# Performance work log

Measured on AMD Instinct MI355X. Metric: run time of the kernel, lower is better.

Reference implementation:

```python
import jax, jax.numpy as jnp
import numpy as np

CLUSTER_NUMBER = 32
SPACING = 2.0 / CLUSTER_NUMBER
GRID = np.linspace(-1.0, 1.0, CLUSTER_NUMBER + 1)  # 33 bin centers, matches torch.linspace


def _eye_bbox_mask(eyes_bool):
    """Replicates the per-sample bounding-box (with 15% pad applied as in the
    original code, including the double-pad quirk on y_max/x_max)."""
    H, W = eyes_bool.shape
    rows_any = jnp.any(eyes_bool, axis=1)
    cols_any = jnp.any(eyes_bool, axis=0)
    ry = jnp.arange(H, dtype=jnp.int32)
    rx = jnp.arange(W, dtype=jnp.int32)
    y_min0 = jnp.min(jnp.where(rows_any, ry, H))
    y_max0 = jnp.max(jnp.where(rows_any, ry, -1))
    x_min0 = jnp.min(jnp.where(cols_any, rx, W))
    x_max0 = jnp.max(jnp.where(cols_any, rx, -1))
    pad_y = (0.15 * (y_max0 - y_min0).astype(jnp.float32)).astype(jnp.int32)
    pad_x = (0.15 * (x_max0 - x_min0).astype(jnp.float32)).astype(jnp.int32)
    y_min = jnp.maximum(0, y_min0 - pad_y)
    y_max = jnp.minimum(H, y_max0 + pad_y)
    x_min = jnp.maximum(0, x_min0 - pad_x)
    x_max = jnp.minimum(W, x_max0 + pad_x)
    # original code pads y_max/x_max a second time
    y_max = jnp.minimum(H - 1, y_max + pad_y)
    x_max = jnp.minimum(W - 1, x_max + pad_x)
    m = ((ry >= y_min) & (ry < y_max))[:, None] & ((rx >= x_min) & (rx < x_max))[None, :]
    has_eyes = jnp.any(eyes_bool)
    return jnp.where(has_eyes, m, False).astype(jnp.float32)


def _region_masks(seg):
    # seg: [B,H,W] int labels
    lips = ((seg == 11) | (seg == 12)).astype(jnp.float32)
    face = (seg == 1).astype(jnp.float32)
    eyes_bool = (seg == 4) | (seg == 5)
    eye_shadow = jax.vmap(_eye_bbox_mask)(eyes_bool)
    return lips, face, eye_shadow


def _soft_hist(img, mask):
    """Masked soft histogram, equivalent to calc_hist over masked pixels.
    result[k] = sum_n m_n*relu(spacing - |g_k - x_n|) / (N * S)  (the *10 cancels).
    img: [B,C,H,W], mask: [B,H,W] -> hist [B,C,K+1], count N [B]."""
    m = mask[:, None]  # [B,1,H,W]
    # small fixed loop over 33 bins keeps the peak intermediate at one [B,C,H,W]
    num = jnp.stack(
        [jnp.sum(jnp.maximum(SPACING - jnp.abs(img - float(g)), 0.0) * m, axis=(2, 3))
         for g in GRID], axis=-1)  # [B,C,K+1]
    N = jnp.sum(mask, axis=(1, 2))  # [B]
    S = jnp.sum(num, axis=-1)       # [B,C]
    denom = N[:, None, None] * S[:, :, None]
    return num / jnp.where(denom > 0, denom, 1.0), N


def reference(gen_makeup, real_makeup, seg_gen, seg_real):
    B, C, H, W = gen_makeup.shape
    gen_regions = _region_masks(seg_gen)
    ref_regions = _region_masks(seg_real)
    weights = (1.0, 0.1, 1.0)  # lips, face, eyes
    total = jnp.zeros((), dtype=gen_makeup.dtype)
    for w, mg, mr in zip(weights, gen_regions, ref_regions):
        hg, ng = _soft_hist(gen_makeup, mg)
        hr, nr = _soft_hist(real_makeup, mr)
        l1 = jnp.mean(jnp.abs(hg - hr), axis=-1)  # [B,C]
        valid = ((ng > 0) & (nr > 0))[:, None]    # empty-region skip
        total = total + w * jnp.sum(jnp.where(valid, l1, 0.0))
    return total / (B * C * 3)


def setup_inputs() -> dict:
    key = jax.random.key(0)
    k1, k2, k3, k4 = jax.random.split(key, 4)
    B, C, H, W = 4, 3, 512, 512
    # images normalized to [-1,1] as in the GAN pipeline
    gen_makeup = jax.random.uniform(k1, (B, C, H, W), dtype=jnp.float32) * 2.0 - 1.0
    real_makeup = jax.random.uniform(k2, (B, C, H, W), dtype=jnp.float32) * 2.0 - 1.0
    seg_gen = jax.random.randint(k3, (B, H, W), 0, 19, dtype=jnp.int32)
    seg_real = jax.random.randint(k4, (B, H, W), 0, 19, dtype=jnp.int32)
    return {"gen_makeup": gen_makeup, "real_makeup": real_makeup,
            "seg_gen": seg_gen, "seg_real": seg_real}
```

## Files before the change

### kernel.cpp

```cpp
#include <hip/hip_runtime.h>

#define HH 512
#define WW 512
#define NB 4
#define NC 3
#define NK 33
#define SPC 0.0625f
#define REP 4
#define NREP 16
#define NCLS 7
#define CLS_SZ (NCLS*NC*NK)
#define GRP_SZ (3*NC*NK)
#define BBOX_CH 64
#define HIST_CH 128
#define NBLK_BBOX (2*NB*BBOX_CH)
#define NBLK_HIST (2*NB*HIST_CH)

#define BBP_OFF    0
#define GCNT_OFF   2056
#define GCNT_SZ    (REP*2*NB*GRP_SZ)
#define GSUM_OFF   (GCNT_OFF + GCNT_SZ)
#define WS_TOTAL   (GSUM_OFF + GCNT_SZ)
#define ZERO_BASE  2048
#define ZERO_SZ    (WS_TOTAL - ZERO_BASE)
#define ZERO_PER   ((ZERO_SZ + NBLK_BBOX - 1) / NBLK_BBOX)

__global__ __launch_bounds__(256) void k_bbox(const int* __restrict__ seg_gen,
                                              const int* __restrict__ seg_real,
                                              int* __restrict__ ws) {
    int bid = blockIdx.x, tid = (int)threadIdx.x;

    int zbase = ZERO_BASE + bid * ZERO_PER;
    for (int i = tid; i < ZERO_PER; i += 256) {
        int idx = zbase + i;
        if (idx < WS_TOTAL) ws[idx] = 0;
    }

    int map = bid / (NB * BBOX_CH);
    int rem = bid % (NB * BBOX_CH);
    int b = rem / BBOX_CH, chunk = rem % BBOX_CH;
    const int4* seg4 = (const int4*)((map == 0 ? seg_gen : seg_real) + b * HH * WW);
    int base4 = chunk * (4096 / 4);

    int4 v[4];
    #pragma unroll
    for (int it = 0; it < 4; ++it) v[it] = seg4[base4 + it * 256 + tid];

    int ymin = HH, ymax = -1, xmin = WW, xmax = -1;
    #pragma unroll
    for (int it = 0; it < 4; ++it) {
        int p0 = (base4 + it * 256 + tid) * 4;
        int h = p0 >> 9, w0 = p0 & (WW - 1);
        int sv[4] = {v[it].x, v[it].y, v[it].z, v[it].w};
        #pragma unroll
        for (int j = 0; j < 4; ++j) {
            int s = sv[j];
            if (s == 4 || s == 5) {
                ymin = min(ymin, h); ymax = max(ymax, h);
                xmin = min(xmin, w0 + j); xmax = max(xmax, w0 + j);
            }
        }
    }
    __shared__ int sy0[256], sy1[256], sx0[256], sx1[256];
    sy0[tid] = ymin; sy1[tid] = ymax; sx0[tid] = xmin; sx1[tid] = xmax;
    __syncthreads();
    for (int off = 128; off > 0; off >>= 1) {
        if (tid < off) {
            sy0[tid] = min(sy0[tid], sy0[tid + off]);
            sy1[tid] = max(sy1[tid], sy1[tid + off]);
            sx0[tid] = min(sx0[tid], sx0[tid + off]);
            sx1[tid] = max(sx1[tid], sx1[tid + off]);
        }
        __syncthreads();
    }
    if (tid == 0)
        ((int4*)ws)[BBP_OFF / 4 + bid] = make_int4(sy0[0], sy1[0], sx0[0], sx1[0]);
}

__global__ __launch_bounds__(256) void k_hist(const float* __restrict__ gen,
                                              const float* __restrict__ realv,
                                              const int* __restrict__ seg_gen,
                                              const int* __restrict__ seg_real,
                                              int* __restrict__ ws) {
    int bid = blockIdx.x, tid = (int)threadIdx.x;
    int map = bid / (NB * HIST_CH);
    int rem = bid % (NB * HIST_CH);
    int b = rem / HIST_CH, chunk = rem % HIST_CH;
    const float* img = (map == 0 ? gen : realv);
    const int* seg = (map == 0 ? seg_gen : seg_real) + b * HH * WW;

    __shared__ unsigned lh[NREP * CLS_SZ];
    __shared__ int sbb[5];

    for (int i = tid; i < NREP * CLS_SZ; i += 256) lh[i] = 0u;

    if (tid < 64) {
        int4 v = ((const int4*)ws)[BBP_OFF / 4 + (map * NB + b) * BBOX_CH + tid];
        #pragma unroll
        for (int off = 32; off > 0; off >>= 1) {
            v.x = min(v.x, __shfl_xor(v.x, off));
            v.y = max(v.y, __shfl_xor(v.y, off));
            v.z = min(v.z, __shfl_xor(v.z, off));
            v.w = max(v.w, __shfl_xor(v.w, off));
        }
        if (tid == 0) {
            int ymin0 = v.x, ymax0 = v.y, xmin0 = v.z, xmax0 = v.w;
            int has = (ymax0 >= 0);
            int pady = (int)(0.15f * (float)(ymax0 - ymin0));
            int padx = (int)(0.15f * (float)(xmax0 - xmin0));
            int ymin = max(0, ymin0 - pady);
            int ymaxv = min(HH, ymax0 + pady);
            int xminv = max(0, xmin0 - padx);
            int xmaxv = min(WW, xmax0 + padx);
            ymaxv = min(HH - 1, ymaxv + pady);
            xmaxv = min(WW - 1, xmaxv + padx);
            sbb[0] = ymin; sbb[1] = ymaxv; sbb[2] = xminv; sbb[3] = xmaxv; sbb[4] = has;
        }
    }
    __syncthreads();
    int bbym = sbb[0], bbyM = sbb[1], bbxm = sbb[2], bbxM = sbb[3], has = sbb[4];

    unsigned* lhr = lh + (tid & (NREP - 1)) * CLS_SZ;
    int q0 = chunk * (2048 / 4) + tid;
    int q1 = q0 + 256;
    const int4* seg4 = (const int4*)seg;
    int4 sA = seg4[q0], sB = seg4[q1];
    const float4* i4 = (const float4*)img + ((size_t)(b * NC) << 16);
    float4 fA0 = i4[(0 << 16) + q0], fA1 = i4[(1 << 16) + q0], fA2 = i4[(2 << 16) + q0];
    float4 fB0 = i4[(0 << 16) + q1], fB1 = i4[(1 << 16) + q1], fB2 = i4[(2 << 16) + q1];

    #pragma unroll
    for (int g = 0; g < 2; ++g) {
        int p = (g == 0 ? q0 : q1) * 4;
        int4 s4 = (g == 0) ? sA : sB;
        float xs0[4], xs1[4], xs2[4];
        { float4 f = (g == 0) ? fA0 : fB0; xs0[0]=f.x; xs0[1]=f.y; xs0[2]=f.z; xs0[3]=f.w; }
        { float4 f = (g == 0) ? fA1 : fB1; xs1[0]=f.x; xs1[1]=f.y; xs1[2]=f.z; xs1[3]=f.w; }
        { float4 f = (g == 0) ? fA2 : fB2; xs2[0]=f.x; xs2[1]=f.y; xs2[2]=f.z; xs2[3]=f.w; }
        int h = p >> 9, w0 = p & (WW - 1);
        bool eyerow = has && (h >= bbym) && (h < bbyM);
        int sv[4] = {s4.x, s4.y, s4.z, s4.w};
        #pragma unroll
        for (int j = 0; j < 4; ++j) {
            int s = sv[j];
            int cls = (int)((s == 11) | (s == 12))
                    | ((int)(s == 1) << 1)
                    | ((int)(eyerow & ((w0 + j) >= bbxm) & ((w0 + j) < bbxM)) << 2);
            if (!cls) continue;
            unsigned* basep = lhr + (cls - 1) * (NC * NK);
            #pragma unroll
            for (int c = 0; c < NC; ++c) {
                float x = (c == 0) ? xs0[j] : (c == 1) ? xs1[j] : xs2[j];
                float t = (x + 1.0f) * 16.0f;
                int k0 = (int)t;
                k0 = min(max(k0, 0), NK - 1);
                float f = t - (float)k0;
                unsigned pk = 0x1000000u | (unsigned)(f * 4096.0f);
                atomicAdd(&basep[c * NK + k0], pk);
            }
        }
    }
    __syncthreads();

    for (int i = tid; i < CLS_SZ; i += 256) {
        unsigned cnt = 0, fq = 0;
        #pragma unroll
        for (int r = 0; r < NREP; ++r) {
            unsigned v = lh[r * CLS_SZ + i];
            cnt += v >> 24;
            fq  += v & 0xFFFFFFu;
        }
        lh[i] = cnt;
        lh[CLS_SZ + i] = fq;
    }
    __syncthreads();

    int rep = bid & (REP - 1);
    unsigned* gcnt = (unsigned*)ws + GCNT_OFF + ((rep * 2 + map) * NB + b) * GRP_SZ;
    float*    gsum = (float*)ws + GSUM_OFF + ((rep * 2 + map) * NB + b) * GRP_SZ;
    const int rcls0[3] = {1, 2, 4};
    for (int i = tid; i < GRP_SZ; i += 256) {
        int r = i / (NC * NK);
        int rest = i % (NC * NK);
        unsigned cnt = 0, fq = 0;
        #pragma unroll
        for (int m = 1; m < 8; ++m) {
            if (m & rcls0[r]) {
                cnt += lh[(m - 1) * (NC * NK) + rest];
                fq  += lh[CLS_SZ + (m - 1) * (NC * NK) + rest];
            }
        }
        if (cnt) {
            atomicAdd(&gcnt[i], cnt);
            atomicAdd(&gsum[i], (float)fq * (1.0f / 4096.0f));
        }
    }
}

#define NITEM (2 * NB * GRP_SZ)
__global__ __launch_bounds__(1024) void k_final(const unsigned* __restrict__ wsu,
                                                const float* __restrict__ wsf,
                                                float* __restrict__ out) {
    int tid = (int)threadIdx.x;
    __shared__ float sC[NITEM], sF[NITEM], sNum[NITEM];
    __shared__ int   sN[2 * NB * 3];
    __shared__ float sS[2 * NB * NC * 3];
    __shared__ double sRed[1024];

    const unsigned* gcntAll = wsu + GCNT_OFF;
    const float*    gsumAll = wsf + GSUM_OFF;
    for (int i = tid; i < NITEM; i += 1024) {
        int mp = i / (NB * GRP_SZ);
        int r2 = i % (NB * GRP_SZ);
        int b2 = r2 / GRP_SZ, idx = r2 % GRP_SZ;
        float C = 0.0f, F = 0.0f;
        #pragma unroll
        for (int rp = 0; rp < REP; ++rp) {
            int off = ((rp * 2 + mp) * NB + b2) * GRP_SZ + idx;
            C += (float)gcntAll[off];
            F += gsumAll[off];
        }
        sC[i] = C; sF[i] = F;
    }
    __syncthreads();
    if (tid < 24) {
        int mp = tid / 12, b2 = (tid / 3) % NB, r = tid % 3;
        const float* p = sC + (mp * NB + b2) * GRP_SZ + r * (NC * NK);
        float n = 0.0f;
        for (int k = 0; k < NK; ++k) n += p[k];
        sN[tid] = (int)(n + 0.5f);
    }
    for (int i = tid; i < NITEM; i += 1024) {
        int k = i % NK;
        float fp = (k > 0) ? sF[i - 1] : 0.0f;
        sNum[i] = fmaxf(SPC * ((sC[i] - sF[i]) + fp), 0.0f);
    }
    __syncthreads();
    if (tid < 72) {
        float s = 0.0f;
        const float* p = sNum + tid * NK;
        for (int k = 0; k < NK; ++k) s += p[k];
        sS[tid] = s;
    }
    __syncthreads();
    double acc = 0.0;
    for (int j = tid; j < NB * GRP_SZ; j += 1024) {
        int b2 = j / GRP_SZ, idx = j % GRP_SZ;
        int r = idx / (NC * NK);
        int c = (idx / NK) % NC;
        int ng = sN[b2 * 3 + r];
        int nr = sN[12 + b2 * 3 + r];
        if (ng > 0 && nr > 0) {
            int g = b2 * 9 + r * 3 + c;
            float dg = (float)ng * sS[g];
            float dr = (float)nr * sS[36 + g];
            dg = (dg > 0.0f) ? dg : 1.0f;
            dr = (dr > 0.0f) ? dr : 1.0f;
            double d = fabs((double)(sNum[j] / dg) - (double)(sNum[NB * GRP_SZ + j] / dr));
            acc += ((r == 1) ? 0.1 : 1.0) * d;
        }
    }
    sRed[tid] = acc;
    __syncthreads();
    for (int off = 512; off > 0; off >>= 1) {
        if (tid < off) sRed[tid] += sRed[tid + off];
        __syncthreads();
    }
    if (tid == 0) out[0] = (float)(sRed[0] / (double)NK / (double)(NB * NC * 3));
}

extern "C" void kernel_launch(void* const* d_in, const int* in_sizes, int n_in,
                              void* d_out, int out_size, void* d_ws, size_t ws_size,
                              hipStream_t stream) {
    const float* gen    = (const float*)d_in[0];
    const float* realv  = (const float*)d_in[1];
    const int* seg_gen  = (const int*)d_in[2];
    const int* seg_real = (const int*)d_in[3];
    int* wsi = (int*)d_ws;

    k_bbox <<<dim3(NBLK_BBOX), dim3(256),  0, stream>>>(seg_gen, seg_real, wsi);
    k_hist <<<dim3(NBLK_HIST), dim3(256),  0, stream>>>(gen, realv, seg_gen, seg_real, wsi);
    k_final<<<dim3(1),         dim3(1024), 0, stream>>>((const unsigned*)d_ws,
                                                        (const float*)d_ws,
                                                        (float*)d_out);
}
```

Baseline: 28.61 us.

## Halve LDS histogram replicas, double bbox blocks, interleave replica partials for vector reads

Cuts the shared-memory histogram replicas from 16 to 8 and repacks counts and fractions into 12/20 bits, with fractions quantized to 512 levels instead of 4096. This shrinks LDS use and the per-block clear and reduction work. The bbox pass now uses twice as many blocks, each reading half the data, so the histogram kernel reads two partials per lane. The global replica partials are interleaved so the final kernel can sum them with single vector loads. The coarser fraction quantization lowers accuracy, and fewer replicas may raise LDS atomic contention.

```diff
diff --git a/kernel.cpp b/kernel.cpp
--- a/kernel.cpp
+++ b/kernel.cpp
@@ -7,21 +7,21 @@
 #define NK 33
 #define SPC 0.0625f
 #define REP 4
-#define NREP 16
+#define NREP 8
 #define NCLS 7
 #define CLS_SZ (NCLS*NC*NK)
 #define GRP_SZ (3*NC*NK)
-#define BBOX_CH 64
+#define BBOX_CH 128
 #define HIST_CH 128
 #define NBLK_BBOX (2*NB*BBOX_CH)
 #define NBLK_HIST (2*NB*HIST_CH)
 
 #define BBP_OFF    0
-#define GCNT_OFF   2056
-#define GCNT_SZ    (REP*2*NB*GRP_SZ)
+#define GCNT_OFF   4096
+#define GCNT_SZ    (2*NB*GRP_SZ*REP)
 #define GSUM_OFF   (GCNT_OFF + GCNT_SZ)
 #define WS_TOTAL   (GSUM_OFF + GCNT_SZ)
-#define ZERO_BASE  2048
+#define ZERO_BASE  GCNT_OFF
 #define ZERO_SZ    (WS_TOTAL - ZERO_BASE)
 #define ZERO_PER   ((ZERO_SZ + NBLK_BBOX - 1) / NBLK_BBOX)
 
@@ -40,18 +40,18 @@
     int rem = bid % (NB * BBOX_CH);
     int b = rem / BBOX_CH, chunk = rem % BBOX_CH;
     const int4* seg4 = (const int4*)((map == 0 ? seg_gen : seg_real) + b * HH * WW);
-    int base4 = chunk * (4096 / 4);
-
-    int4 v[4];
-    #pragma unroll
-    for (int it = 0; it < 4; ++it) v[it] = seg4[base4 + it * 256 + tid];
+    int base4 = chunk * 512;
+
+    int4 v0 = seg4[base4 + tid];
+    int4 v1 = seg4[base4 + 256 + tid];
 
     int ymin = HH, ymax = -1, xmin = WW, xmax = -1;
     #pragma unroll
-    for (int it = 0; it < 4; ++it) {
+    for (int it = 0; it < 2; ++it) {
         int p0 = (base4 + it * 256 + tid) * 4;
         int h = p0 >> 9, w0 = p0 & (WW - 1);
-        int sv[4] = {v[it].x, v[it].y, v[it].z, v[it].w};
+        int4 v = (it == 0) ? v0 : v1;
+        int sv[4] = {v.x, v.y, v.z, v.w};
         #pragma unroll
         for (int j = 0; j < 4; ++j) {
             int s = sv[j];
@@ -95,16 +95,19 @@
     for (int i = tid; i < NREP * CLS_SZ; i += 256) lh[i] = 0u;
 
     if (tid < 64) {
-        int4 v = ((const int4*)ws)[BBP_OFF / 4 + (map * NB + b) * BBOX_CH + tid];
+        const int4* bbp = (const int4*)ws + BBP_OFF / 4 + (map * NB + b) * BBOX_CH;
+        int4 a = bbp[tid], c = bbp[tid + 64];
+        a.x = min(a.x, c.x); a.y = max(a.y, c.y);
+        a.z = min(a.z, c.z); a.w = max(a.w, c.w);
         #pragma unroll
         for (int off = 32; off > 0; off >>= 1) {
-            v.x = min(v.x, __shfl_xor(v.x, off));
-            v.y = max(v.y, __shfl_xor(v.y, off));
-            v.z = min(v.z, __shfl_xor(v.z, off));
-            v.w = max(v.w, __shfl_xor(v.w, off));
+            a.x = min(a.x, __shfl_xor(a.x, off));
+            a.y = max(a.y, __shfl_xor(a.y, off));
+            a.z = min(a.z, __shfl_xor(a.z, off));
+            a.w = max(a.w, __shfl_xor(a.w, off));
         }
         if (tid == 0) {
-            int ymin0 = v.x, ymax0 = v.y, xmin0 = v.z, xmax0 = v.w;
+            int ymin0 = a.x, ymax0 = a.y, xmin0 = a.z, xmax0 = a.w;
             int has = (ymax0 >= 0);
             int pady = (int)(0.15f * (float)(ymax0 - ymin0));
             int padx = (int)(0.15f * (float)(xmax0 - xmin0));
@@ -121,7 +124,7 @@
     int bbym = sbb[0], bbyM = sbb[1], bbxm = sbb[2], bbxM = sbb[3], has = sbb[4];
 
     unsigned* lhr = lh + (tid & (NREP - 1)) * CLS_SZ;
-    int q0 = chunk * (2048 / 4) + tid;
+    int q0 = chunk * 512 + tid;
     int q1 = q0 + 256;
     const int4* seg4 = (const int4*)seg;
     int4 sA = seg4[q0], sB = seg4[q1];
@@ -155,7 +158,7 @@
                 int k0 = (int)t;
                 k0 = min(max(k0, 0), NK - 1);
                 float f = t - (float)k0;
-                unsigned pk = 0x1000000u | (unsigned)(f * 4096.0f);
+                unsigned pk = 0x100000u | (unsigned)(f * 512.0f);
                 atomicAdd(&basep[c * NK + k0], pk);
             }
         }
@@ -167,8 +170,8 @@
         #pragma unroll
         for (int r = 0; r < NREP; ++r) {
             unsigned v = lh[r * CLS_SZ + i];
-            cnt += v >> 24;
-            fq  += v & 0xFFFFFFu;
+            cnt += v >> 20;
+            fq  += v & 0xFFFFFu;
         }
         lh[i] = cnt;
         lh[CLS_SZ + i] = fq;
@@ -176,8 +179,8 @@
     __syncthreads();
 
     int rep = bid & (REP - 1);
-    unsigned* gcnt = (unsigned*)ws + GCNT_OFF + ((rep * 2 + map) * NB + b) * GRP_SZ;
-    float*    gsum = (float*)ws + GSUM_OFF + ((rep * 2 + map) * NB + b) * GRP_SZ;
+    unsigned* gcnt = (unsigned*)ws + GCNT_OFF + (map * NB + b) * GRP_SZ * REP;
+    float*    gsum = (float*)ws + GSUM_OFF + (map * NB + b) * GRP_SZ * REP;
     const int rcls0[3] = {1, 2, 4};
     for (int i = tid; i < GRP_SZ; i += 256) {
         int r = i / (NC * NK);
@@ -191,8 +194,8 @@
             }
         }
         if (cnt) {
-            atomicAdd(&gcnt[i], cnt);
-            atomicAdd(&gsum[i], (float)fq * (1.0f / 4096.0f));
+            atomicAdd(&gcnt[i * REP + rep], cnt);
+            atomicAdd(&gsum[i * REP + rep], (float)fq * (1.0f / 512.0f));
         }
     }
 }
@@ -210,17 +213,10 @@
     const unsigned* gcntAll = wsu + GCNT_OFF;
     const float*    gsumAll = wsf + GSUM_OFF;
     for (int i = tid; i < NITEM; i += 1024) {
-        int mp = i / (NB * GRP_SZ);
-        int r2 = i % (NB * GRP_SZ);
-        int b2 = r2 / GRP_SZ, idx = r2 % GRP_SZ;
-        float C = 0.0f, F = 0.0f;
-        #pragma unroll
-        for (int rp = 0; rp < REP; ++rp) {
-            int off = ((rp * 2 + mp) * NB + b2) * GRP_SZ + idx;
-            C += (float)gcntAll[off];
-            F += gsumAll[off];
-        }
-        sC[i] = C; sF[i] = F;
+        uint4  u  = *(const uint4*)&gcntAll[i * REP];
+        float4 fv = *(const float4*)&gsumAll[i * REP];
+        sC[i] = (float)(u.x + u.y + u.z + u.w);
+        sF[i] = fv.x + fv.y + fv.z + fv.w;
     }
     __syncthreads();
     if (tid < 24) {
```

Measured after the change: 30.26 us. +5.8%, slower.
